# Performance work log

Hardware: AMD Instinct MI355X
Metric: run time of the kernel (lower is better)

The kernel has to match this reference:

```python
import jax, jax.numpy as jnp
import numpy as np

X_DIM = 40
N_BATCH = 65536


def _circ_conv1d(x, W, b, pad):
    # x: [N, C_in, L], W: [C_out, C_in, K] (torch layout), circular padding
    if pad > 0:
        x = jnp.pad(x, ((0, 0), (0, 0), (pad, pad)), mode='wrap')
    y = jax.lax.conv_general_dilated(x, W, window_strides=(1,), padding='VALID',
                                     dimension_numbers=('NCH', 'OIH', 'NCH'))
    return y + b[None, :, None]


def setup_inputs() -> dict:
    key = jax.random.key(0)
    ks = jax.random.split(key, 9)
    u = jax.random.normal(ks[0], (N_BATCH, X_DIM), dtype=jnp.float32)
    coeff = jax.random.normal(ks[1], (18,), dtype=jnp.float32) * 0.1
    # Conv1d params, torch layout [out_ch, in_ch, kernel], kaiming-ish scale
    W1 = jax.random.normal(ks[2], (72, 1, 5), dtype=jnp.float32) * (1.0 / np.sqrt(1 * 5))
    b1 = jax.random.normal(ks[3], (72,), dtype=jnp.float32) * 0.05
    W2 = jax.random.normal(ks[4], (37, 48, 5), dtype=jnp.float32) * (1.0 / np.sqrt(48 * 5))
    b2 = jax.random.normal(ks[5], (37,), dtype=jnp.float32) * 0.05
    W3 = jax.random.normal(ks[6], (1, 37, 1), dtype=jnp.float32) * (1.0 / np.sqrt(37))
    b3 = jax.random.normal(ks[7], (1,), dtype=jnp.float32) * 0.05
    t = jnp.zeros((1,), dtype=jnp.float32)  # unused by the module, kept for signature fidelity
    return {"t": t, "u": u, "coeff": coeff, "W1": W1, "b1": b1,
            "W2": W2, "b2": b2, "W3": W3, "b3": b3}


def reference(t, u, coeff, W1, b1, W2, b2, W3, b3):
    # circular neighbor gathers: index_select with (i+k)%D == roll by -k
    u_m2 = jnp.roll(u, 2, axis=-1)
    u_m1 = jnp.roll(u, 1, axis=-1)
    u_p1 = jnp.roll(u, -1, axis=-1)
    u_p2 = jnp.roll(u, -2, axis=-1)
    feats = jnp.stack([
        jnp.ones_like(u),
        u_m2, u_m1, u, u_p1, u_p2,
        u_m2 ** 2, u_m1 ** 2, u ** 2, u_p1 ** 2, u_p2 ** 2,
        u_m2 * u_m1, u_m1 * u, u * u_p1, u_p1 * u_p2,
        u_m2 * u, u_m1 * u_p1, u * u_p2,
    ], axis=-1)  # [N, D, 18]
    out1 = feats @ coeff  # [N, D]

    x = u[:, None, :]  # [N, 1, D]
    h = jax.nn.relu(_circ_conv1d(x, W1, b1, 2))  # [N, 72, D]
    h = jnp.concatenate([h[:, :24], h[:, 24:48] * h[:, 48:]], axis=1)  # [N, 48, D]
    h = jax.nn.relu(_circ_conv1d(h, W2, b2, 2))  # [N, 37, D]
    out2 = _circ_conv1d(h, W3, b3, 0)[:, 0, :]  # [N, D]
    return out1 + out2
```

## Files before the change

kernel.cpp:

```cpp
#include <hip/hip_runtime.h>
#include <hip/hip_bf16.h>

typedef short s16x8 __attribute__((ext_vector_type(8)));
typedef short s16x4 __attribute__((ext_vector_type(4)));
typedef float f32x4 __attribute__((ext_vector_type(4)));

#define TB 8
#define NBG 16
#define HALO 46
#define GSTRIDE 2216
#define USTRIDE 50
#define NT 3
#define GT_SHORTS (TB * GSTRIDE)

__device__ __forceinline__ unsigned short f2bf(float f) {
    unsigned int u = __float_as_uint(f);
    u += 0x7fff + ((u >> 16) & 1);
    return (unsigned short)(u >> 16);
}

__device__ __forceinline__ unsigned int pk_bf16(float lo, float hi) {
    float2 f; f.x = lo; f.y = hi;
    __hip_bfloat162 h = __float22bfloat162_rn(f);
    union { __hip_bfloat162 b; unsigned int u; } c;
    c.b = h;
    return c.u;
}

__global__ __launch_bounds__(256, 2) void lorenz96_fused(
    const float* __restrict__ u,
    const float* __restrict__ coeff,
    const float* __restrict__ W1,
    const float* __restrict__ b1,
    const float* __restrict__ W2,
    const float* __restrict__ b2,
    const float* __restrict__ W3,
    const float* __restrict__ b3,
    float* __restrict__ out)
{
    __shared__ __align__(16) unsigned short gtile[2][GT_SHORTS];
    __shared__ __align__(16) float u_sbuf[2][TB * USTRIDE];

    unsigned short* B_lds = &gtile[0][0];

    const int t    = threadIdx.x;
    const int lane = t & 63;
    const int wave = t >> 6;
    const int quad = lane >> 4;
    const int l15  = lane & 15;

    const int b0_block = blockIdx.x * (TB * NBG);

    for (int g = t; g < NT * 8 * 64; g += 256) {
        int lg = g & 63;
        int ks = (g >> 6) & 7;
        int nt = g >> 9;
        int o  = nt * 16 + (lg & 15);
        int kb = ks * 32 + (lg >> 4) * 8;
        s16x8 pack = {0, 0, 0, 0, 0, 0, 0, 0};
        #pragma unroll
        for (int j = 0; j < 8; ++j) {
            int k = kb + j;
            if (o < 37) {
                if (k < 240) {
                    int c = k % 48, tap = k / 48;
                    pack[j] = (short)f2bf(W2[o * 240 + c * 5 + tap]);
                } else if (k == 240) {
                    pack[j] = (short)f2bf(b2[o]);
                }
            }
        }
        *(s16x8*)&B_lds[g * 8] = pack;
    }

    s16x8 aW1[5];
    {
        int chs[5];
        chs[0] = l15; chs[1] = 16 + l15; chs[2] = 32 + l15;
        chs[3] = (l15 >= 8) ? 40 + l15 : -1;
        chs[4] = 56 + l15;
        #pragma unroll
        for (int mt = 0; mt < 5; ++mt) {
            s16x8 a = {0, 0, 0, 0, 0, 0, 0, 0};
            int ch = chs[mt];
            if (quad == 0 && ch >= 0) {
                #pragma unroll
                for (int j = 0; j < 5; ++j) a[j] = (short)f2bf(W1[ch * 5 + j]);
                a[5] = (short)f2bf(b1[ch]);
            }
            aW1[mt] = a;
        }
    }

    float w3v[NT][4];
    #pragma unroll
    for (int nt = 0; nt < NT; ++nt)
        #pragma unroll
        for (int r = 0; r < 4; ++r) {
            int o = nt * 16 + quad * 4 + r;
            w3v[nt][r] = (o < 37) ? W3[o] : 0.f;
        }
    const float b3v = b3[0];
    float cf[18];
    #pragma unroll
    for (int i = 0; i < 18; ++i) cf[i] = coeff[i];

    s16x8 aW2[NT][8];
    float pv_q = 0.f, pv_4 = 0.f;

    auto prestage_u = [&](int grp) {
        for (int idx = t; idx < TB * USTRIDE; idx += 256) {
            int b = idx / USTRIDE, k = idx - b * USTRIDE;
            int gi = k + 36; gi -= (gi >= 40) ? 40 : 0; gi -= (gi >= 40) ? 40 : 0;
            u_sbuf[grp & 1][idx] = u[(size_t)(b0_block + grp * TB + b) * 40 + gi];
        }
    };

    auto poly1 = [&](const float* u_s, int m) -> float {
        int p = m >> 3, b = m & 7;
        const float* us = &u_s[b * USTRIDE + p];
        float um2 = us[2], um1 = us[3], u0 = us[4], up1 = us[5], up2 = us[6];
        return cf[0] + cf[1]*um2 + cf[2]*um1 + cf[3]*u0 + cf[4]*up1 + cf[5]*up2
             + cf[6]*um2*um2 + cf[7]*um1*um1 + cf[8]*u0*u0 + cf[9]*up1*up1 + cf[10]*up2*up2
             + cf[11]*um2*um1 + cf[12]*um1*u0 + cf[13]*u0*up1 + cf[14]*up1*up2
             + cf[15]*um2*u0 + cf[16]*um1*up1 + cf[17]*u0*up2;
    };

    auto poly = [&](int grp) {
        const float* u_s = u_sbuf[grp & 1];
        pv_q = poly1(u_s, (wave + 4 * quad) * 16 + l15);
        pv_4 = poly1(u_s, (wave + 16) * 16 + l15);
    };

    auto phase2 = [&](int grp) {
        const float* u_s = u_sbuf[grp & 1];
        unsigned short* gt = &gtile[grp & 1][0];
        #pragma unroll
        for (int i = 0; i < 6; ++i) {
            const int ct = wave + 4 * i;
            if (ct > 22) continue;
            const int col = ct * 16 + l15;
            const int b = col & 7, h = col >> 3;
            s16x8 bU = {0, 0, 0, 0, 0, 0, 0, 0};
            if (quad == 0) {
                const float* us = &u_s[b * USTRIDE + h];
                union { s16x8 v; unsigned int w[4]; } bu;
                bu.w[0] = pk_bf16(us[0], us[1]);
                bu.w[1] = pk_bf16(us[2], us[3]);
                bu.w[2] = pk_bf16(us[4], 1.0f);
                bu.w[3] = 0;
                bU = bu.v;
            }
            f32x4 a0 = {0.f,0.f,0.f,0.f}, a1 = a0, a2 = a0, a3 = a0, a4 = a0;
            a0 = __builtin_amdgcn_mfma_f32_16x16x32_bf16(aW1[0], bU, a0, 0, 0, 0);
            a1 = __builtin_amdgcn_mfma_f32_16x16x32_bf16(aW1[1], bU, a1, 0, 0, 0);
            a2 = __builtin_amdgcn_mfma_f32_16x16x32_bf16(aW1[2], bU, a2, 0, 0, 0);
            a3 = __builtin_amdgcn_mfma_f32_16x16x32_bf16(aW1[3], bU, a3, 0, 0, 0);
            a4 = __builtin_amdgcn_mfma_f32_16x16x32_bf16(aW1[4], bU, a4, 0, 0, 0);
            float v0[4], v1[4], v2[4];
            #pragma unroll
            for (int r = 0; r < 4; ++r) {
                v0[r] = fmaxf(a0[r], 0.f);
                v1[r] = fmaxf(a1[r], 0.f);
                if (quad >= 2) v1[r] *= fmaxf(a3[r], 0.f);
                v2[r] = fmaxf(a2[r], 0.f) * fmaxf(a4[r], 0.f);
            }
            union { s16x4 v; unsigned int w[2]; } w0, w1, w2;
            w0.w[0] = pk_bf16(v0[0], v0[1]); w0.w[1] = pk_bf16(v0[2], v0[3]);
            w1.w[0] = pk_bf16(v1[0], v1[1]); w1.w[1] = pk_bf16(v1[2], v1[3]);
            w2.w[0] = pk_bf16(v2[0], v2[1]); w2.w[1] = pk_bf16(v2[2], v2[3]);
            unsigned short* gp = &gt[b * GSTRIDE + h * 48 + quad * 4];
            *(s16x4*)(gp)      = w0.v;
            *(s16x4*)(gp + 16) = w1.v;
            *(s16x4*)(gp + 32) = w2.v;
        }
    };

    auto p3_tile = [&](int i, const unsigned short* gt, int b0) {
        const int mt = wave + 4 * i;
        const int m  = mt * 16 + l15;
        const int p  = m >> 3, b = m & 7;
        const unsigned short* gbase = &gt[b * GSTRIDE + p * 48 + quad * 8];
        s16x8 bg[8];
        #pragma unroll
        for (int ks = 0; ks < 8; ++ks) bg[ks] = *(const s16x8*)(gbase + ks * 32);
        {
            s16x8 b7 = bg[7];
            if (quad == 2) b7[0] = (short)0x3F80;
            bg[7] = b7;
        }
        f32x4 c0 = {0.f,0.f,0.f,0.f}, c1 = c0, c2 = c0;
        #pragma unroll
        for (int ks = 0; ks < 8; ++ks) {
            c0 = __builtin_amdgcn_mfma_f32_16x16x32_bf16(aW2[0][ks], bg[ks], c0, 0, 0, 0);
            c1 = __builtin_amdgcn_mfma_f32_16x16x32_bf16(aW2[1][ks], bg[ks], c1, 0, 0, 0);
            c2 = __builtin_amdgcn_mfma_f32_16x16x32_bf16(aW2[2][ks], bg[ks], c2, 0, 0, 0);
        }
        float s = 0.f;
        #pragma unroll
        for (int r = 0; r < 4; ++r) {
            s += fmaxf(c0[r], 0.f) * w3v[0][r];
            s += fmaxf(c1[r], 0.f) * w3v[1][r];
            s += fmaxf(c2[r], 0.f) * w3v[2][r];
        }
        s += __shfl_xor(s, 16, 64);
        s += __shfl_xor(s, 32, 64);
        const float pv = (i < 4) ? pv_q : pv_4;
        const bool  st = (i < 4) ? (quad == i) : (quad == 0);
        if (st) {
            out[(size_t)(b0 + (l15 & 7)) * 40 + 2 * mt + (l15 >> 3)] = s + b3v + pv;
        }
    };

    prestage_u(0);
    __syncthreads();

    #pragma unroll
    for (int nt = 0; nt < NT; ++nt)
        #pragma unroll
        for (int ks = 0; ks < 8; ++ks)
            aW2[nt][ks] = *(const s16x8*)&B_lds[((nt * 8 + ks) * 64 + lane) * 8];

    poly(0);
    prestage_u(1);
    __syncthreads();

    phase2(0);
    __syncthreads();

    for (int g = 0; g < NBG; ++g) {
        const int b0 = b0_block + g * TB;
        const unsigned short* gt = &gtile[g & 1][0];

        #pragma unroll
        for (int i = 0; i < 5; ++i) p3_tile(i, gt, b0);

        if (g + 1 < NBG) {
            poly(g + 1);
            phase2(g + 1);
            if (g + 2 < NBG) prestage_u(g + 2);
            __syncthreads();
        }
    }
}

extern "C" void kernel_launch(void* const* d_in, const int* in_sizes, int n_in,
                              void* d_out, int out_size, void* d_ws, size_t ws_size,
                              hipStream_t stream) {
    const float* u     = (const float*)d_in[1];
    const float* coeff = (const float*)d_in[2];
    const float* W1    = (const float*)d_in[3];
    const float* b1    = (const float*)d_in[4];
    const float* W2    = (const float*)d_in[5];
    const float* b2    = (const float*)d_in[6];
    const float* W3    = (const float*)d_in[7];
    const float* b3    = (const float*)d_in[8];
    float* out = (float*)d_out;

    const int n_batch = in_sizes[1] / 40;
    const int grid = n_batch / (TB * NBG);
    lorenz96_fused<<<grid, 256, 0, stream>>>(u, coeff, W1, b1, W2, b2, W3, b3, out);
}
```

Baseline: 181.5 us.

## Raise occupancy to three blocks per CU with persistent grid and reduced LDS/registers

After: 190.2 us. 4.7% more time.

```diff
diff --git a/kernel.cpp b/kernel.cpp
--- a/kernel.cpp
+++ b/kernel.cpp
@@ -6,12 +6,12 @@
 typedef float f32x4 __attribute__((ext_vector_type(4)));
 
 #define TB 8
-#define NBG 16
 #define HALO 46
 #define GSTRIDE 2216
 #define USTRIDE 50
 #define NT 3
 #define GT_SHORTS (TB * GSTRIDE)
+#define GRID 768
 
 __device__ __forceinline__ unsigned short f2bf(float f) {
     unsigned int u = __float_as_uint(f);
@@ -27,7 +27,11 @@
     return c.u;
 }
 
-__global__ __launch_bounds__(256, 2) void lorenz96_fused(
+__device__ __forceinline__ float sload(const float* p) {
+    return __uint_as_float(__builtin_amdgcn_readfirstlane(__float_as_uint(*p)));
+}
+
+__global__ __launch_bounds__(256, 3) void lorenz96_fused(
     const float* __restrict__ u,
     const float* __restrict__ coeff,
     const float* __restrict__ W1,
@@ -36,12 +40,14 @@
     const float* __restrict__ b2,
     const float* __restrict__ W3,
     const float* __restrict__ b3,
-    float* __restrict__ out)
+    float* __restrict__ out,
+    int n_batch)
 {
-    __shared__ __align__(16) unsigned short gtile[2][GT_SHORTS];
+    __shared__ __align__(16) unsigned short gtile[GT_SHORTS];
+    __shared__ __align__(16) unsigned short W2s[8 * 64 * 8];
     __shared__ __align__(16) float u_sbuf[2][TB * USTRIDE];
 
-    unsigned short* B_lds = &gtile[0][0];
+    unsigned short* B_lds = &gtile[0];
 
     const int t    = threadIdx.x;
     const int lane = t & 63;
@@ -49,7 +55,13 @@
     const int quad = lane >> 4;
     const int l15  = lane & 15;
 
-    const int b0_block = blockIdx.x * (TB * NBG);
+    const int TG  = n_batch / TB;
+    const int nb  = (int)gridDim.x;
+    const int qq  = TG / nb, rr = TG - qq * nb;
+    const int bid = (int)blockIdx.x;
+    const int g_start  = bid * qq + (bid < rr ? bid : rr);
+    const int n_my     = qq + (bid < rr ? 1 : 0);
+    const int b0_block = g_start * TB;
 
     for (int g = t; g < NT * 8 * 64; g += 256) {
         int lg = g & 63;
@@ -70,7 +82,8 @@
                 }
             }
         }
-        *(s16x8*)&B_lds[g * 8] = pack;
+        if (nt < 2) *(s16x8*)&B_lds[g * 8] = pack;
+        else        *(s16x8*)&W2s[(g - 1024) * 8] = pack;
     }
 
     s16x8 aW1[5];
@@ -100,19 +113,19 @@
             int o = nt * 16 + quad * 4 + r;
             w3v[nt][r] = (o < 37) ? W3[o] : 0.f;
         }
-    const float b3v = b3[0];
+    const float b3v = sload(b3);
     float cf[18];
     #pragma unroll
-    for (int i = 0; i < 18; ++i) cf[i] = coeff[i];
-
-    s16x8 aW2[NT][8];
+    for (int i = 0; i < 18; ++i) cf[i] = sload(&coeff[i]);
+
+    s16x8 aW2[2][8];
     float pv_q = 0.f, pv_4 = 0.f;
 
-    auto prestage_u = [&](int grp) {
+    auto prestage_u = [&](int gi) {
         for (int idx = t; idx < TB * USTRIDE; idx += 256) {
             int b = idx / USTRIDE, k = idx - b * USTRIDE;
-            int gi = k + 36; gi -= (gi >= 40) ? 40 : 0; gi -= (gi >= 40) ? 40 : 0;
-            u_sbuf[grp & 1][idx] = u[(size_t)(b0_block + grp * TB + b) * 40 + gi];
+            int g2 = k + 36; g2 -= (g2 >= 40) ? 40 : 0; g2 -= (g2 >= 40) ? 40 : 0;
+            u_sbuf[gi & 1][idx] = u[(size_t)(b0_block + gi * TB + b) * 40 + g2];
         }
     };
 
@@ -126,15 +139,15 @@
              + cf[15]*um2*u0 + cf[16]*um1*up1 + cf[17]*u0*up2;
     };
 
-    auto poly = [&](int grp) {
-        const float* u_s = u_sbuf[grp & 1];
+    auto poly = [&](int gi) {
+        const float* u_s = u_sbuf[gi & 1];
         pv_q = poly1(u_s, (wave + 4 * quad) * 16 + l15);
         pv_4 = poly1(u_s, (wave + 16) * 16 + l15);
     };
 
-    auto phase2 = [&](int grp) {
-        const float* u_s = u_sbuf[grp & 1];
-        unsigned short* gt = &gtile[grp & 1][0];
+    auto phase2 = [&](int gi) {
+        const float* u_s = u_sbuf[gi & 1];
+        unsigned short* gt = &gtile[0];
         #pragma unroll
         for (int i = 0; i < 6; ++i) {
             const int ct = wave + 4 * i;
@@ -176,25 +189,33 @@
         }
     };
 
-    auto p3_tile = [&](int i, const unsigned short* gt, int b0) {
-        const int mt = wave + 4 * i;
+    auto p3_tile = [&](int ti, int b0) {
+        const unsigned short* gt = &gtile[0];
+        const int mt = wave + 4 * ti;
         const int m  = mt * 16 + l15;
         const int p  = m >> 3, b = m & 7;
         const unsigned short* gbase = &gt[b * GSTRIDE + p * 48 + quad * 8];
-        s16x8 bg[8];
-        #pragma unroll
-        for (int ks = 0; ks < 8; ++ks) bg[ks] = *(const s16x8*)(gbase + ks * 32);
-        {
-            s16x8 b7 = bg[7];
-            if (quad == 2) b7[0] = (short)0x3F80;
-            bg[7] = b7;
-        }
         f32x4 c0 = {0.f,0.f,0.f,0.f}, c1 = c0, c2 = c0;
-        #pragma unroll
-        for (int ks = 0; ks < 8; ++ks) {
-            c0 = __builtin_amdgcn_mfma_f32_16x16x32_bf16(aW2[0][ks], bg[ks], c0, 0, 0, 0);
-            c1 = __builtin_amdgcn_mfma_f32_16x16x32_bf16(aW2[1][ks], bg[ks], c1, 0, 0, 0);
-            c2 = __builtin_amdgcn_mfma_f32_16x16x32_bf16(aW2[2][ks], bg[ks], c2, 0, 0, 0);
+        s16x8 aw2n = *(const s16x8*)&W2s[lane * 8];
+        #pragma unroll
+        for (int half = 0; half < 2; ++half) {
+            s16x8 bg[4];
+            #pragma unroll
+            for (int j = 0; j < 4; ++j) bg[j] = *(const s16x8*)(gbase + (half * 4 + j) * 32);
+            if (half == 1) {
+                s16x8 b7 = bg[3];
+                if (quad == 2) b7[0] = (short)0x3F80;
+                bg[3] = b7;
+            }
+            #pragma unroll
+            for (int j = 0; j < 4; ++j) {
+                const int ks = half * 4 + j;
+                s16x8 cur = aw2n;
+                if (ks < 7) aw2n = *(const s16x8*)&W2s[((ks + 1) * 64 + lane) * 8];
+                c0 = __builtin_amdgcn_mfma_f32_16x16x32_bf16(aW2[0][ks], bg[j], c0, 0, 0, 0);
+                c1 = __builtin_amdgcn_mfma_f32_16x16x32_bf16(aW2[1][ks], bg[j], c1, 0, 0, 0);
+                c2 = __builtin_amdgcn_mfma_f32_16x16x32_bf16(cur,        bg[j], c2, 0, 0, 0);
+            }
         }
         float s = 0.f;
         #pragma unroll
@@ -205,8 +226,8 @@
         }
         s += __shfl_xor(s, 16, 64);
         s += __shfl_xor(s, 32, 64);
-        const float pv = (i < 4) ? pv_q : pv_4;
-        const bool  st = (i < 4) ? (quad == i) : (quad == 0);
+        const float pv = (ti < 4) ? pv_q : pv_4;
+        const bool  st = (ti < 4) ? (quad == ti) : (quad == 0);
         if (st) {
             out[(size_t)(b0 + (l15 & 7)) * 40 + 2 * mt + (l15 >> 3)] = s + b3v + pv;
         }
@@ -216,29 +237,29 @@
     __syncthreads();
 
     #pragma unroll
-    for (int nt = 0; nt < NT; ++nt)
+    for (int nt = 0; nt < 2; ++nt)
         #pragma unroll
         for (int ks = 0; ks < 8; ++ks)
             aW2[nt][ks] = *(const s16x8*)&B_lds[((nt * 8 + ks) * 64 + lane) * 8];
 
     poly(0);
-    prestage_u(1);
+    if (n_my > 1) prestage_u(1);
     __syncthreads();
 
     phase2(0);
     __syncthreads();
 
-    for (int g = 0; g < NBG; ++g) {
-        const int b0 = b0_block + g * TB;
-        const unsigned short* gt = &gtile[g & 1][0];
-
-        #pragma unroll
-        for (int i = 0; i < 5; ++i) p3_tile(i, gt, b0);
-
-        if (g + 1 < NBG) {
-            poly(g + 1);
-            phase2(g + 1);
-            if (g + 2 < NBG) prestage_u(g + 2);
+    for (int gidx = 0; gidx < n_my; ++gidx) {
+        const int b0 = b0_block + gidx * TB;
+
+        #pragma unroll
+        for (int ti = 0; ti < 5; ++ti) p3_tile(ti, b0);
+
+        if (gidx + 1 < n_my) {
+            __syncthreads();
+            poly(gidx + 1);
+            phase2(gidx + 1);
+            if (gidx + 2 < n_my) prestage_u(gidx + 2);
             __syncthreads();
         }
     }
@@ -258,6 +279,8 @@
     float* out = (float*)d_out;
 
     const int n_batch = in_sizes[1] / 40;
-    const int grid = n_batch / (TB * NBG);
-    lorenz96_fused<<<grid, 256, 0, stream>>>(u, coeff, W1, b1, W2, b2, W3, b3, out);
-}
+    int grid = GRID;
+    const int tg = n_batch / TB;
+    if (grid > tg) grid = tg;
+    lorenz96_fused<<<grid, 256, 0, stream>>>(u, coeff, W1, b1, W2, b2, W3, b3, out, n_batch);
+}
```

## Issue next u-tile global loads early and overlap polynomial with MFMA phase

Applied to the files above, without the earlier changes.

Result: no change. 180.1 us (-0.8%).

```diff
diff --git a/kernel.cpp b/kernel.cpp
--- a/kernel.cpp
+++ b/kernel.cpp
@@ -25,6 +25,10 @@
     union { __hip_bfloat162 b; unsigned int u; } c;
     c.b = h;
     return c.u;
+}
+
+__device__ __forceinline__ float sload(const float* p) {
+    return __uint_as_float(__builtin_amdgcn_readfirstlane(__float_as_uint(*p)));
 }
 
 __global__ __launch_bounds__(256, 2) void lorenz96_fused(
@@ -100,13 +104,14 @@
             int o = nt * 16 + quad * 4 + r;
             w3v[nt][r] = (o < 37) ? W3[o] : 0.f;
         }
-    const float b3v = b3[0];
+    const float b3v = sload(b3);
     float cf[18];
     #pragma unroll
-    for (int i = 0; i < 18; ++i) cf[i] = coeff[i];
+    for (int i = 0; i < 18; ++i) cf[i] = sload(&coeff[i]);
 
     s16x8 aW2[NT][8];
     float pv_q = 0.f, pv_4 = 0.f;
+    float st_v0 = 0.f, st_v1 = 0.f;
 
     auto prestage_u = [&](int grp) {
         for (int idx = t; idx < TB * USTRIDE; idx += 256) {
@@ -114,6 +119,26 @@
             int gi = k + 36; gi -= (gi >= 40) ? 40 : 0; gi -= (gi >= 40) ? 40 : 0;
             u_sbuf[grp & 1][idx] = u[(size_t)(b0_block + grp * TB + b) * 40 + gi];
         }
+    };
+
+    auto prestage_issue = [&](int grp) {
+        {
+            int idx = t;
+            int b = idx / USTRIDE, k = idx - b * USTRIDE;
+            int gi = k + 36; gi -= (gi >= 40) ? 40 : 0; gi -= (gi >= 40) ? 40 : 0;
+            st_v0 = u[(size_t)(b0_block + grp * TB + b) * 40 + gi];
+        }
+        if (t + 256 < TB * USTRIDE) {
+            int idx = t + 256;
+            int b = idx / USTRIDE, k = idx - b * USTRIDE;
+            int gi = k + 36; gi -= (gi >= 40) ? 40 : 0; gi -= (gi >= 40) ? 40 : 0;
+            st_v1 = u[(size_t)(b0_block + grp * TB + b) * 40 + gi];
+        }
+    };
+
+    auto prestage_commit = [&](int grp) {
+        u_sbuf[grp & 1][t] = st_v0;
+        if (t + 256 < TB * USTRIDE) u_sbuf[grp & 1][t + 256] = st_v1;
     };
 
     auto poly1 = [&](const float* u_s, int m) -> float {
@@ -126,15 +151,9 @@
              + cf[15]*um2*u0 + cf[16]*um1*up1 + cf[17]*u0*up2;
     };
 
-    auto poly = [&](int grp) {
-        const float* u_s = u_sbuf[grp & 1];
-        pv_q = poly1(u_s, (wave + 4 * quad) * 16 + l15);
-        pv_4 = poly1(u_s, (wave + 16) * 16 + l15);
-    };
-
-    auto phase2 = [&](int grp) {
-        const float* u_s = u_sbuf[grp & 1];
-        unsigned short* gt = &gtile[grp & 1][0];
+    auto phase2 = [&](int gi) {
+        const float* u_s = u_sbuf[gi & 1];
+        unsigned short* gt = &gtile[gi & 1][0];
         #pragma unroll
         for (int i = 0; i < 6; ++i) {
             const int ct = wave + 4 * i;
@@ -221,7 +240,11 @@
         for (int ks = 0; ks < 8; ++ks)
             aW2[nt][ks] = *(const s16x8*)&B_lds[((nt * 8 + ks) * 64 + lane) * 8];
 
-    poly(0);
+    {
+        const float* u_s = u_sbuf[0];
+        pv_q = poly1(u_s, (wave + 4 * quad) * 16 + l15);
+        pv_4 = poly1(u_s, (wave + 16) * 16 + l15);
+    }
     prestage_u(1);
     __syncthreads();
 
@@ -232,13 +255,22 @@
         const int b0 = b0_block + g * TB;
         const unsigned short* gt = &gtile[g & 1][0];
 
+        if (g + 2 < NBG) prestage_issue(g + 2);
+
+        float tq = 0.f, t4 = 0.f;
+        if (g + 1 < NBG) {
+            const float* u_s = u_sbuf[(g + 1) & 1];
+            tq = poly1(u_s, (wave + 4 * quad) * 16 + l15);
+            t4 = poly1(u_s, (wave + 16) * 16 + l15);
+        }
+
         #pragma unroll
         for (int i = 0; i < 5; ++i) p3_tile(i, gt, b0);
 
         if (g + 1 < NBG) {
-            poly(g + 1);
             phase2(g + 1);
-            if (g + 2 < NBG) prestage_u(g + 2);
+            if (g + 2 < NBG) prestage_commit(g + 2);
+            pv_q = tq; pv_4 = t4;
             __syncthreads();
         }
     }
```
